# Optimization experiments

Measured on AMD Instinct MI355X. Metric: run time of the kernel, lower is better.

Reference implementation:

```python
import jax, jax.numpy as jnp
import numpy as np

B, NV, NC, D, GD = 4, 2048, 8192, 64, 8


def setup_inputs() -> dict:
    key = jax.random.key(0)
    ks = jax.random.split(key, 16)
    f32 = jnp.float32
    rn = lambda k, s, fan: (jax.random.normal(k, s, dtype=f32) / np.float32(np.sqrt(fan)))
    raw = jax.random.randint(ks[0], (B, NC, NV), 0, 20)
    c_mat = jnp.where(raw == 0, -1.0, jnp.where(raw == 1, 1.0, 0.0)).astype(f32)
    v_mat = jnp.transpose(c_mat, (0, 2, 1))  # [B, NV, NC]
    variables = jax.random.normal(ks[1], (B, NV, D), dtype=f32)
    ground_vars = jax.random.normal(ks[2], (B, NV, GD), dtype=f32)
    # learned params
    c_block = rn(ks[3], (2, D, D), D)  # pos/neg literal projections (clause side)
    v_block = rn(ks[4], (2, D, D), D)  # pos/neg literal projections (variable side)
    vb = jax.random.normal(ks[5], (D,), dtype=f32)
    cb = jax.random.normal(ks[6], (D,), dtype=f32)
    Wg = rn(ks[7], (D, GD + D), GD + D)  # ground combiner Linear(concat) -> D
    bg = jnp.zeros((D,), f32)
    Wz = rn(ks[8], (D, D), D); Uz = rn(ks[9], (D, D), D); bz = jnp.zeros((D,), f32)
    Wr = rn(ks[10], (D, D), D); Ur = rn(ks[11], (D, D), D); br = jnp.zeros((D,), f32)
    Wh = rn(ks[12], (D, D), D); Uh = rn(ks[13], (D, D), D); bh = jnp.zeros((D,), f32)
    return dict(variables=variables, ground_vars=ground_vars, c_mat=c_mat, v_mat=v_mat,
                c_block=c_block, v_block=v_block, vb=vb, cb=cb, Wg=Wg, bg=bg,
                Wz=Wz, Uz=Uz, bz=bz, Wr=Wr, Ur=Ur, br=br, Wh=Wh, Uh=Uh, bh=bh)


def reference(variables, ground_vars, c_mat, v_mat, c_block, v_block, vb, cb,
              Wg, bg, Wz, Uz, bz, Wr, Ur, br, Wh, Uh, bh):
    b, nv, d = variables.shape
    v = variables.reshape(-1, d)  # [B*NV, D]
    # clause-side literal projections: bmm(c_block, v^T)^T == v @ c_block[i]^T
    pos_vars = (v @ c_block[0].T).reshape(b, nv, d)
    neg_vars = (v @ c_block[1].T).reshape(b, nv, d)
    pos_cmat = jnp.clip(c_mat, 0.0, 1.0)
    neg_cmat = -jnp.clip(c_mat, -1.0, 0.0)
    c = (jnp.einsum('bcv,bvd->bcd', pos_cmat, pos_vars)
         + jnp.einsum('bcv,bvd->bcd', neg_cmat, neg_vars))  # [B, NC, D]
    c = jax.nn.relu(c + cb)
    cv = c.reshape(-1, d)  # [B*NC, D]
    pos_cvars = (cv @ v_block[0].T).reshape(b, -1, d)
    neg_cvars = (cv @ v_block[1].T).reshape(b, -1, d)
    pos_vmat = jnp.clip(v_mat, 0.0, 1.0)
    neg_vmat = -jnp.clip(v_mat, -1.0, 0.0)
    nv_msg = (jnp.einsum('bvc,bcd->bvd', pos_vmat, pos_cvars)
              + jnp.einsum('bvc,bcd->bvd', neg_vmat, neg_cvars))  # [B, NV, D]
    v_emb = jax.nn.relu(nv_msg + vb).reshape(-1, d)
    # ground combiner: tanh(Linear(concat(ground, v_emb)))
    g = ground_vars.reshape(-1, ground_vars.shape[-1])
    av = jnp.tanh(jnp.concatenate([g, v_emb], axis=-1) @ Wg.T + bg)
    # GRU update against previous variable embeddings
    prev = v
    z = jax.nn.sigmoid(av @ Wz.T + prev @ Uz.T + bz)
    r = jax.nn.sigmoid(av @ Wr.T + prev @ Ur.T + br)
    h_tilda = jnp.tanh(av @ Wh.T + (r * prev) @ Uh.T + bh)
    h = (1.0 - z) * prev + z * h_tilda
    return h.reshape(b, nv * d, 1)
```

## Files before the change

kernel.cpp:

```cpp
#include <hip/hip_runtime.h>
#include <hip/hip_bf16.h>
#include <stdint.h>

#define NBATCH 4
#define NV 2048
#define NC 8192
#define DD 64

typedef __attribute__((ext_vector_type(8))) short s16x8;
typedef __attribute__((ext_vector_type(4))) float fx4;
typedef __attribute__((ext_vector_type(8))) unsigned short u16x8;
typedef __attribute__((ext_vector_type(4))) int i32x4;
typedef __attribute__((ext_vector_type(2))) unsigned int u32x2;

static __device__ __forceinline__ void gload_lds16(const void* g, void* l) {
    __builtin_amdgcn_global_load_lds(
        (const __attribute__((address_space(1))) unsigned int*)g,
        (__attribute__((address_space(3))) unsigned int*)l, 16, 0, 0);
}

__global__ __launch_bounds__(256) void k_front(
    const float* __restrict__ cmat, unsigned short* __restrict__ comp,
    const float* __restrict__ vars, const float* __restrict__ cblk,
    char* __restrict__ qsh, char* __restrict__ qsl,
    char* __restrict__ qdh, char* __restrict__ qdl)
{
    __shared__ __align__(16) char pool[41472];
    int blk = blockIdx.x;
    int t = threadIdx.x;
    if (blk < 4096) {
        char (*sb)[260] = (char(*)[260])pool;
        int tv = blk & 7;
        int rg = (blk >> 3) & 127;
        int b = blk >> 10;
        int wv = t >> 6, l = t & 63;
        int crow0 = rg * 64;
        const float* src = cmat + (size_t)b * NC * NV + (size_t)crow0 * NV + tv * 256;
        #pragma unroll 4
        for (int rr = 0; rr < 16; ++rr) {
            int r = wv * 16 + rr;
            fx4 x = *(const fx4*)(src + (size_t)r * NV + l * 4);
            unsigned int pk = ((unsigned int)((int)x[0] & 0xFF))
                            | (((unsigned int)((int)x[1] & 0xFF)) << 8)
                            | (((unsigned int)((int)x[2] & 0xFF)) << 16)
                            | (((unsigned int)((int)x[3] & 0xFF)) << 24);
            *(unsigned int*)&sb[r][l * 4] = pk;
        }
        __syncthreads();
        unsigned short* cbp = comp + ((size_t)b * 256 + tv * 32) * NC + crow0;
        #pragma unroll
        for (int it = 0; it < 8; ++it) {
            int idx = it * 256 + t;
            int v8l = idx >> 6, r = idx & 63;
            unsigned int lo = *(const unsigned int*)&sb[r][v8l * 8];
            unsigned int hi = *(const unsigned int*)&sb[r][v8l * 8 + 4];
            unsigned int c0 = 0;
            #pragma unroll
            for (int i = 0; i < 4; ++i) c0 |= ((lo >> (8 * i)) & 3u) << (2 * i);
            #pragma unroll
            for (int i = 0; i < 4; ++i) c0 |= ((hi >> (8 * i)) & 3u) << (8 + 2 * i);
            cbp[(size_t)v8l * NC + r] = (unsigned short)c0;
        }
    } else {
        float (*sv)[64] = (float(*)[64])pool;
        float (*scb)[65] = (float(*)[65])(pool + 8192);
        int blk2 = blk - 4096;
        int b = blk2 >> 6, ch = blk2 & 63;
        const float* vsrc = vars + ((size_t)b * NV + (size_t)ch * 32) * DD;
        for (int i = t; i < 32 * 64; i += 256) sv[i >> 6][i & 63] = vsrc[i];
        for (int i = t; i < 2 * 64 * 64; i += 256) {
            int pn = i >> 12, dout = (i >> 6) & 63, k = i & 63;
            scb[pn * 64 + k][dout] = cblk[i];
        }
        __syncthreads();
        int ks = t >> 6, dout = t & 63;
        unsigned int wsh[2] = {0, 0}, wsl[2] = {0, 0}, wdh[2] = {0, 0}, wdl[2] = {0, 0};
        #pragma unroll
        for (int c8 = 0; c8 < 8; ++c8) {
            int vloc = ks * 8 + c8;
            float ap = 0.f, an = 0.f;
            for (int k = 0; k < 64; ++k) {
                float vv = sv[vloc][k];
                ap += vv * scb[k][dout];
                an += vv * scb[64 + k][dout];
            }
            float s = (ap + an) * 0.5f, dv = (ap - an) * 0.5f;
            int qs_ = (int)rintf(s * 4096.f);
            int qd_ = (int)rintf(dv * 4096.f);
            qs_ = min(max(qs_, -32511), 32511);
            qd_ = min(max(qd_, -32511), 32511);
            int sh = (qs_ + 128) >> 8, sl = qs_ - (sh << 8);
            int dh = (qd_ + 128) >> 8, dl = qd_ - (dh << 8);
            int w = c8 >> 2, sft = (c8 & 3) * 8;
            wsh[w] |= (unsigned int)(sh & 0xFF) << sft;
            wsl[w] |= (unsigned int)(sl & 0xFF) << sft;
            wdh[w] |= (unsigned int)(dh & 0xFF) << sft;
            wdl[w] |= (unsigned int)(dl & 0xFF) << sft;
        }
        int kc = ch >> 1;
        int lg = ((ch & 1) << 1) | (ks >> 1);
        size_t off = (((size_t)(b * 32 + kc) * 64 + dout) * 4 + lg) * 16 + (ks & 1) * 8;
        *(u32x2*)(qsh + off) = (u32x2){wsh[0], wsh[1]};
        *(u32x2*)(qsl + off) = (u32x2){wsl[0], wsl[1]};
        *(u32x2*)(qdh + off) = (u32x2){wdh[0], wdh[1]};
        *(u32x2*)(qdl + off) = (u32x2){wdl[0], wdl[1]};
    }
}

__global__ __launch_bounds__(256, 2) void k_phaseA(
    const unsigned short* __restrict__ comp,
    const char* __restrict__ qsh, const char* __restrict__ qsl,
    const char* __restrict__ qdh, const char* __restrict__ qdl,
    const float* __restrict__ cb, const float* __restrict__ vblk,
    char* __restrict__ csh, char* __restrict__ csl,
    char* __restrict__ cdh, char* __restrict__ cdl)
{
    __shared__ __align__(16) char pool[50176];
    int blk = blockIdx.x;
    int b = blk & 3;
    int rg = blk >> 2;
    int t = threadIdx.x;
    int wv = t >> 6, l = t & 63, lr = l & 15, lg = l >> 4;
    int crow0 = rg * 64;
    int crow = crow0 + wv * 16 + lr;
    const unsigned short* compb = comp + (size_t)b * 256 * NC;

    i32x4 ahi[4], alo[4];
    #pragma unroll
    for (int n = 0; n < 4; ++n) { ahi[n] = (i32x4){0,0,0,0}; alo[n] = (i32x4){0,0,0,0}; }

    {
        size_t gb = ((size_t)(b * 32)) * 4096 + (size_t)t * 16;
        char* lp = pool + t * 16;
        gload_lds16(qsh + gb, lp);
        gload_lds16(qsl + gb, lp + 4096);
        gload_lds16(qdh + gb, lp + 8192);
        gload_lds16(qdl + gb, lp + 12288);
    }
    unsigned int u0, u1, u0n, u1n;
    u0 = compb[(size_t)(lg * 2) * NC + crow];
    u1 = compb[(size_t)(lg * 2 + 1) * NC + crow];
    __syncthreads();

    int cur = 0;
    #pragma unroll 1
    for (int kc = 0; kc < 32; ++kc) {
        if (kc < 31) {
            size_t gb = ((size_t)(b * 32 + kc + 1)) * 4096 + (size_t)t * 16;
            char* lp = pool + (cur ^ 1) * 16384 + t * 16;
            gload_lds16(qsh + gb, lp);
            gload_lds16(qsl + gb, lp + 4096);
            gload_lds16(qdh + gb, lp + 8192);
            gload_lds16(qdl + gb, lp + 12288);
            size_t v8 = (size_t)((kc + 1) * 8 + lg * 2);
            u0n = compb[v8 * NC + crow];
            u1n = compb[(v8 + 1) * NC + crow];
        }
        i32x4 Asgn, Aabs;
        #pragma unroll
        for (int w = 0; w < 4; ++w) {
            unsigned int wg = 0;
            #pragma unroll
            for (int jj = 0; jj < 4; ++jj) {
                int j = w * 4 + jj;
                unsigned int u = (j < 8) ? u0 : u1;
                int c = ((int)(u << (30 - 2 * (j & 7)))) >> 30;
                wg |= ((unsigned int)c & 0xFFu) << (8 * jj);
            }
            Asgn[w] = (int)wg;
        }
        #pragma unroll
        for (int w = 0; w < 4; ++w) Aabs[w] = Asgn[w] & 0x01010101;
        const char* bufp = pool + cur * 16384;
        #pragma unroll
        for (int n = 0; n < 4; ++n) {
            int boff = ((n * 16 + lr) * 4 + lg) * 16;
            i32x4 Bsh = *(const i32x4*)(bufp + boff);
            i32x4 Bsl = *(const i32x4*)(bufp + 4096 + boff);
            i32x4 Bdh = *(const i32x4*)(bufp + 8192 + boff);
            i32x4 Bdl = *(const i32x4*)(bufp + 12288 + boff);
            ahi[n] = __builtin_amdgcn_mfma_i32_16x16x64_i8(Aabs, Bsh, ahi[n], 0, 0, 0);
            ahi[n] = __builtin_amdgcn_mfma_i32_16x16x64_i8(Asgn, Bdh, ahi[n], 0, 0, 0);
            alo[n] = __builtin_amdgcn_mfma_i32_16x16x64_i8(Aabs, Bsl, alo[n], 0, 0, 0);
            alo[n] = __builtin_amdgcn_mfma_i32_16x16x64_i8(Asgn, Bdl, alo[n], 0, 0, 0);
        }
        if (kc < 31) { u0 = u0n; u1 = u1n; }
        __syncthreads();
        cur ^= 1;
    }

    int* sbC = (int*)pool;
    float* sbCf = (float*)pool;
    float* svb = (float*)(pool + 64 * 66 * 4);
    #pragma unroll
    for (int n = 0; n < 4; ++n)
        #pragma unroll
        for (int r = 0; r < 4; ++r)
            sbC[(wv * 16 + lg * 4 + r) * 66 + n * 16 + lr] = ahi[n][r] * 256 + alo[n][r];
    for (int i = t * 4; i < 8192; i += 1024) {
        fx4 g4 = *(const fx4*)(vblk + i);
        int pn = i >> 12, dout = (i >> 6) & 63, k0 = i & 63;
        #pragma unroll
        for (int jj = 0; jj < 4; ++jj) svb[(pn * 64 + k0 + jj) * 65 + dout] = g4[jj];
    }
    __syncthreads();
    for (int idx = t; idx < 4096; idx += 256) {
        int row = idx >> 6, k = idx & 63;
        float f = (float)sbC[row * 66 + k] * (1.0f / 4096.0f) + cb[k];
        sbCf[row * 66 + k] = fmaxf(f, 0.f);
    }
    __syncthreads();
    int dout = l;
    float ap[16], an[16];
    #pragma unroll
    for (int c8 = 0; c8 < 16; ++c8) { ap[c8] = 0.f; an[c8] = 0.f; }
    for (int k = 0; k < 64; ++k) {
        float w0 = svb[k * 65 + dout];
        float w1 = svb[(64 + k) * 65 + dout];
        #pragma unroll
        for (int c8 = 0; c8 < 16; ++c8) {
            float rc = sbCf[(wv * 16 + c8) * 66 + k];
            ap[c8] += rc * w0;
            an[c8] += rc * w1;
        }
    }
    unsigned int osh[4] = {0,0,0,0}, osl[4] = {0,0,0,0}, odh[4] = {0,0,0,0}, odl[4] = {0,0,0,0};
    #pragma unroll
    for (int c8 = 0; c8 < 16; ++c8) {
        float s = (ap[c8] + an[c8]) * 0.5f, dv = (ap[c8] - an[c8]) * 0.5f;
        int q_s = (int)rintf(s * 512.f);
        int q_d = (int)rintf(dv * 512.f);
        q_s = min(max(q_s, -32511), 32511);
        q_d = min(max(q_d, -32511), 32511);
        int sh = (q_s + 128) >> 8, sl = q_s - (sh << 8);
        int dh = (q_d + 128) >> 8, dl = q_d - (dh << 8);
        int w = c8 >> 2, sft = (c8 & 3) * 8;
        osh[w] |= (unsigned int)(sh & 0xFF) << sft;
        osl[w] |= (unsigned int)(sl & 0xFF) << sft;
        odh[w] |= (unsigned int)(dh & 0xFF) << sft;
        odl[w] |= (unsigned int)(dl & 0xFF) << sft;
    }
    size_t off = (((size_t)(b * 128 + rg) * 64 + dout) * 64) + wv * 16;
    *(i32x4*)(csh + off) = (i32x4){(int)osh[0], (int)osh[1], (int)osh[2], (int)osh[3]};
    *(i32x4*)(csl + off) = (i32x4){(int)osl[0], (int)osl[1], (int)osl[2], (int)osl[3]};
    *(i32x4*)(cdh + off) = (i32x4){(int)odh[0], (int)odh[1], (int)odh[2], (int)odh[3]};
    *(i32x4*)(cdl + off) = (i32x4){(int)odl[0], (int)odl[1], (int)odl[2], (int)odl[3]};
}

__global__ __launch_bounds__(256, 4) void k_phaseB(
    const unsigned short* __restrict__ comp,
    const char* __restrict__ csh, const char* __restrict__ csl,
    const char* __restrict__ cdh, const char* __restrict__ cdl,
    float* __restrict__ npart)
{
    __shared__ char lds[2][16384];
    int blk = blockIdx.x;
    int combo = blk & 63;
    int rg = blk >> 6;
    int b = combo >> 4;
    int q = combo & 15;
    int t = threadIdx.x;
    int wv = t >> 6, l = t & 63, lr = l & 15, lg = l >> 4;
    int v0 = rg * 128 + wv * 32;
    const unsigned short* compb = comp + (size_t)b * 256 * NC;
    int sh_ = 2 * (lr & 7);
    const unsigned short* cp0 = compb + (size_t)((v0 + lr) >> 3) * NC + q * 512 + lg * 16;
    const unsigned short* cp1 = compb + (size_t)((v0 + 16 + lr) >> 3) * NC + q * 512 + lg * 16;
    const size_t cbase = ((size_t)(b * 128 + q * 8)) * 4096;

    i32x4 ahi[2][4], alo[2][4];
    #pragma unroll
    for (int i = 0; i < 2; ++i)
        #pragma unroll
        for (int j = 0; j < 4; ++j) { ahi[i][j] = (i32x4){0,0,0,0}; alo[i][j] = (i32x4){0,0,0,0}; }

    {
        size_t gb = cbase + (size_t)t * 16;
        char* lp = &lds[0][t * 16];
        gload_lds16(csh + gb, lp);
        gload_lds16(csl + gb, lp + 4096);
        gload_lds16(cdh + gb, lp + 8192);
        gload_lds16(cdl + gb, lp + 12288);
    }
    __syncthreads();

    int cur = 0;
    #pragma unroll 1
    for (int cc = 0; cc < 8; ++cc) {
        u16x8 u00 = *(const u16x8*)(cp0 + cc * 64);
        u16x8 u01 = *(const u16x8*)(cp0 + cc * 64 + 8);
        u16x8 u10 = *(const u16x8*)(cp1 + cc * 64);
        u16x8 u11 = *(const u16x8*)(cp1 + cc * 64 + 8);
        if (cc < 7) {
            size_t gb = cbase + (size_t)(cc + 1) * 4096 + (size_t)t * 16;
            char* lp = &lds[cur ^ 1][t * 16];
            gload_lds16(csh + gb, lp);
            gload_lds16(csl + gb, lp + 4096);
            gload_lds16(cdh + gb, lp + 8192);
            gload_lds16(cdl + gb, lp + 12288);
        }
        i32x4 Asgn[2], Aabs[2];
        #pragma unroll
        for (int rt = 0; rt < 2; ++rt) {
            u16x8 ua = rt ? u10 : u00;
            u16x8 ub = rt ? u11 : u01;
            i32x4 sg;
            #pragma unroll
            for (int g = 0; g < 4; ++g) {
                unsigned int wg = 0;
                #pragma unroll
                for (int jj = 0; jj < 4; ++jj) {
                    int j = g * 4 + jj;
                    unsigned int code = ((unsigned int)(j < 8 ? ua[j & 7] : ub[j & 7]) >> sh_) & 3u;
                    unsigned int byt = (code == 3u) ? 0xFFu : code;
                    wg |= byt << (jj * 8);
                }
                sg[g] = (int)wg;
            }
            Asgn[rt] = sg;
            i32x4 ab;
            #pragma unroll
            for (int g = 0; g < 4; ++g) ab[g] = sg[g] & 0x01010101;
            Aabs[rt] = ab;
        }
        const char* bufp = &lds[cur][0];
        #pragma unroll
        for (int n = 0; n < 4; ++n) {
            int boff = ((n * 16 + lr) * 4 + lg) * 16;
            i32x4 Bsh = *(const i32x4*)(bufp + boff);
            i32x4 Bsl = *(const i32x4*)(bufp + 4096 + boff);
            i32x4 Bdh = *(const i32x4*)(bufp + 8192 + boff);
            i32x4 Bdl = *(const i32x4*)(bufp + 12288 + boff);
            #pragma unroll
            for (int rt = 0; rt < 2; ++rt) {
                ahi[rt][n] = __builtin_amdgcn_mfma_i32_16x16x64_i8(Aabs[rt], Bsh, ahi[rt][n], 0, 0, 0);
                ahi[rt][n] = __builtin_amdgcn_mfma_i32_16x16x64_i8(Asgn[rt], Bdh, ahi[rt][n], 0, 0, 0);
                alo[rt][n] = __builtin_amdgcn_mfma_i32_16x16x64_i8(Aabs[rt], Bsl, alo[rt][n], 0, 0, 0);
                alo[rt][n] = __builtin_amdgcn_mfma_i32_16x16x64_i8(Asgn[rt], Bdl, alo[rt][n], 0, 0, 0);
            }
        }
        __syncthreads();
        cur ^= 1;
    }
    float* dst = npart + (((size_t)q * NBATCH + b) * NV + v0) * DD;
    #pragma unroll
    for (int rt = 0; rt < 2; ++rt)
        #pragma unroll
        for (int n = 0; n < 4; ++n)
            #pragma unroll
            for (int r = 0; r < 4; ++r) {
                float v = (float)(ahi[rt][n][r] * 256 + alo[rt][n][r]) * (1.0f / 512.0f);
                dst[(size_t)(rt * 16 + lg * 4 + r) * DD + n * 16 + lr] = v;
            }
}

__global__ __launch_bounds__(512) void k_gru(
    const float* __restrict__ npart, const float* __restrict__ vars,
    const float* __restrict__ gv, const float* __restrict__ vb,
    const float* __restrict__ Wg, const float* __restrict__ bg,
    const float* __restrict__ Wz, const float* __restrict__ Uz, const float* __restrict__ bz,
    const float* __restrict__ Wr, const float* __restrict__ Ur, const float* __restrict__ brr,
    const float* __restrict__ Wh, const float* __restrict__ Uh, const float* __restrict__ bh,
    float* __restrict__ out)
{
    __shared__ float sWg[72][65];
    __shared__ float sWz[64][65], sUz[64][65];
    __shared__ float sWr[64][65], sUr[64][65];
    __shared__ float sWh[64][65], sUh[64][65];
    __shared__ float scat[8][72];
    __shared__ float sprev[8][64];
    __shared__ float sav[8][64];
    __shared__ float srp[8][64];
    int t = threadIdx.x;
    for (int i = t * 4; i < 4608; i += 2048) {
        fx4 g4 = *(const fx4*)(Wg + i);
        int dout = i / 72, j = i - dout * 72;
        #pragma unroll
        for (int jj = 0; jj < 4; ++jj) sWg[j + jj][dout] = g4[jj];
    }
    for (int i = t * 4; i < 4096; i += 2048) {
        int dout = i >> 6, k = i & 63;
        fx4 a;
        a = *(const fx4*)(Wz + i);
        #pragma unroll
        for (int jj = 0; jj < 4; ++jj) sWz[k + jj][dout] = a[jj];
        a = *(const fx4*)(Uz + i);
        #pragma unroll
        for (int jj = 0; jj < 4; ++jj) sUz[k + jj][dout] = a[jj];
        a = *(const fx4*)(Wr + i);
        #pragma unroll
        for (int jj = 0; jj < 4; ++jj) sWr[k + jj][dout] = a[jj];
        a = *(const fx4*)(Ur + i);
        #pragma unroll
        for (int jj = 0; jj < 4; ++jj) sUr[k + jj][dout] = a[jj];
        a = *(const fx4*)(Wh + i);
        #pragma unroll
        for (int jj = 0; jj < 4; ++jj) sWh[k + jj][dout] = a[jj];
        a = *(const fx4*)(Uh + i);
        #pragma unroll
        for (int jj = 0; jj < 4; ++jj) sUh[k + jj][dout] = a[jj];
    }
    int rr = t >> 6, dout = t & 63;
    const size_t qs = (size_t)NBATCH * NV * DD;
    #pragma unroll 1
    for (int it = 0; it < 4; ++it) {
        size_t row = (size_t)blockIdx.x * 32 + it * 8 + rr;
        float prev = vars[row * 64 + dout];
        float ve = vb[dout];
        #pragma unroll
        for (int s = 0; s < 16; ++s) ve += npart[(size_t)s * qs + row * 64 + dout];
        ve = fmaxf(ve, 0.f);
        scat[rr][8 + dout] = ve;
        if (dout < 8) scat[rr][dout] = gv[row * 8 + dout];
        sprev[rr][dout] = prev;
        __syncthreads();
        float a = bg[dout];
        for (int j = 0; j < 72; ++j) a += scat[rr][j] * sWg[j][dout];
        float av = 1.f - 2.f / (__expf(2.f * a) + 1.f);
        sav[rr][dout] = av;
        __syncthreads();
        float zi = bz[dout], ri = brr[dout], hwa = 0.f;
        for (int k = 0; k < 64; ++k) {
            float ak = sav[rr][k], pk = sprev[rr][k];
            zi += ak * sWz[k][dout] + pk * sUz[k][dout];
            ri += ak * sWr[k][dout] + pk * sUr[k][dout];
            hwa += ak * sWh[k][dout];
        }
        float z = 1.f / (1.f + __expf(-zi));
        float rgate = 1.f / (1.f + __expf(-ri));
        srp[rr][dout] = rgate * prev;
        __syncthreads();
        float hin = bh[dout] + hwa;
        for (int k = 0; k < 64; ++k) hin += srp[rr][k] * sUh[k][dout];
        float ht = 1.f - 2.f / (__expf(2.f * hin) + 1.f);
        out[row * 64 + dout] = (1.f - z) * prev + z * ht;
        __syncthreads();
    }
}

extern "C" void kernel_launch(void* const* d_in, const int* in_sizes, int n_in,
                              void* d_out, int out_size, void* d_ws, size_t ws_size,
                              hipStream_t stream) {
    (void)in_sizes; (void)n_in; (void)out_size; (void)ws_size;
    const float* vars = (const float*)d_in[0];
    const float* gv   = (const float*)d_in[1];
    const float* cmat = (const float*)d_in[2];
    const float* cblk = (const float*)d_in[4];
    const float* vblk = (const float*)d_in[5];
    const float* vb   = (const float*)d_in[6];
    const float* cb   = (const float*)d_in[7];
    const float* Wg   = (const float*)d_in[8];
    const float* bg   = (const float*)d_in[9];
    const float* Wz   = (const float*)d_in[10];
    const float* Uz   = (const float*)d_in[11];
    const float* bz   = (const float*)d_in[12];
    const float* Wr   = (const float*)d_in[13];
    const float* Ur   = (const float*)d_in[14];
    const float* br_  = (const float*)d_in[15];
    const float* Wh   = (const float*)d_in[16];
    const float* Uh   = (const float*)d_in[17];
    const float* bh   = (const float*)d_in[18];
    float* out = (float*)d_out;

    char* w = (char*)d_ws;
    const size_t MB = 1024 * 1024;
    char* qsh = w + 0 * MB;
    char* qsl = w + 1 * MB;
    char* qdh = w + 2 * MB;
    char* qdl = w + 3 * MB;
    char* csh = w + 4 * MB;
    char* csl = w + 6 * MB;
    char* cdh = w + 8 * MB;
    char* cdl = w + 10 * MB;
    float* npart         = (float*)(w + 12 * MB);
    unsigned short* comp = (unsigned short*)(w + 44 * MB);

    k_front<<<4352, 256, 0, stream>>>(cmat, comp, vars, cblk, qsh, qsl, qdh, qdl);
    k_phaseA<<<512, 256, 0, stream>>>(comp, qsh, qsl, qdh, qdl, cb, vblk,
                                      csh, csl, cdh, cdl);
    k_phaseB<<<1024, 256, 0, stream>>>(comp, csh, csl, cdh, cdl, npart);
    k_gru<<<256, 512, 0, stream>>>(npart, vars, gv, vb, Wg, bg,
                                   Wz, Uz, bz, Wr, Ur, br_, Wh, Uh, bh, out);
}
```

Baseline: 152.2 us.

## Use two waves per phaseA block, each computing two 16-row MFMA tiles

Phase A blocks drop from four waves to two, and each wave now handles 32 clause rows as two 16-row MFMA tiles. Each B fragment read from LDS then feeds twice as many MFMAs, and each thread issues twice as many global-to-LDS loads. The aim is fewer LDS reads per MFMA and less barrier cost per unit of work. In exchange, per-thread register pressure rises (double accumulators, 32-row epilogue arrays) and each block has fewer waves to hide latency.

Result: slower. 165.7 us (+8.9%).

```diff
diff --git a/kernel.cpp b/kernel.cpp
--- a/kernel.cpp
+++ b/kernel.cpp
@@ -107,7 +107,7 @@
     }
 }
 
-__global__ __launch_bounds__(256, 2) void k_phaseA(
+__global__ __launch_bounds__(128) void k_phaseA(
     const unsigned short* __restrict__ comp,
     const char* __restrict__ qsh, const char* __restrict__ qsl,
     const char* __restrict__ qdh, const char* __restrict__ qdl,
@@ -122,24 +122,31 @@
     int t = threadIdx.x;
     int wv = t >> 6, l = t & 63, lr = l & 15, lg = l >> 4;
     int crow0 = rg * 64;
-    int crow = crow0 + wv * 16 + lr;
+    int crow[2];
+    crow[0] = crow0 + wv * 32 + lr;
+    crow[1] = crow0 + wv * 32 + 16 + lr;
     const unsigned short* compb = comp + (size_t)b * 256 * NC;
 
-    i32x4 ahi[4], alo[4];
-    #pragma unroll
-    for (int n = 0; n < 4; ++n) { ahi[n] = (i32x4){0,0,0,0}; alo[n] = (i32x4){0,0,0,0}; }
+    i32x4 ahi[2][4], alo[2][4];
+    #pragma unroll
+    for (int rt = 0; rt < 2; ++rt)
+        #pragma unroll
+        for (int n = 0; n < 4; ++n) { ahi[rt][n] = (i32x4){0,0,0,0}; alo[rt][n] = (i32x4){0,0,0,0}; }
 
     {
         size_t gb = ((size_t)(b * 32)) * 4096 + (size_t)t * 16;
         char* lp = pool + t * 16;
-        gload_lds16(qsh + gb, lp);
-        gload_lds16(qsl + gb, lp + 4096);
-        gload_lds16(qdh + gb, lp + 8192);
-        gload_lds16(qdl + gb, lp + 12288);
-    }
-    unsigned int u0, u1, u0n, u1n;
-    u0 = compb[(size_t)(lg * 2) * NC + crow];
-    u1 = compb[(size_t)(lg * 2 + 1) * NC + crow];
+        gload_lds16(qsh + gb, lp);             gload_lds16(qsh + gb + 2048, lp + 2048);
+        gload_lds16(qsl + gb, lp + 4096);      gload_lds16(qsl + gb + 2048, lp + 6144);
+        gload_lds16(qdh + gb, lp + 8192);      gload_lds16(qdh + gb + 2048, lp + 10240);
+        gload_lds16(qdl + gb, lp + 12288);     gload_lds16(qdl + gb + 2048, lp + 14336);
+    }
+    unsigned int u0[2], u1[2], u0n[2], u1n[2];
+    #pragma unroll
+    for (int rt = 0; rt < 2; ++rt) {
+        u0[rt] = compb[(size_t)(lg * 2) * NC + crow[rt]];
+        u1[rt] = compb[(size_t)(lg * 2 + 1) * NC + crow[rt]];
+    }
     __syncthreads();
 
     int cur = 0;
@@ -148,29 +155,35 @@
         if (kc < 31) {
             size_t gb = ((size_t)(b * 32 + kc + 1)) * 4096 + (size_t)t * 16;
             char* lp = pool + (cur ^ 1) * 16384 + t * 16;
-            gload_lds16(qsh + gb, lp);
-            gload_lds16(qsl + gb, lp + 4096);
-            gload_lds16(qdh + gb, lp + 8192);
-            gload_lds16(qdl + gb, lp + 12288);
+            gload_lds16(qsh + gb, lp);             gload_lds16(qsh + gb + 2048, lp + 2048);
+            gload_lds16(qsl + gb, lp + 4096);      gload_lds16(qsl + gb + 2048, lp + 6144);
+            gload_lds16(qdh + gb, lp + 8192);      gload_lds16(qdh + gb + 2048, lp + 10240);
+            gload_lds16(qdl + gb, lp + 12288);     gload_lds16(qdl + gb + 2048, lp + 14336);
             size_t v8 = (size_t)((kc + 1) * 8 + lg * 2);
-            u0n = compb[v8 * NC + crow];
-            u1n = compb[(v8 + 1) * NC + crow];
-        }
-        i32x4 Asgn, Aabs;
-        #pragma unroll
-        for (int w = 0; w < 4; ++w) {
-            unsigned int wg = 0;
-            #pragma unroll
-            for (int jj = 0; jj < 4; ++jj) {
-                int j = w * 4 + jj;
-                unsigned int u = (j < 8) ? u0 : u1;
-                int c = ((int)(u << (30 - 2 * (j & 7)))) >> 30;
-                wg |= ((unsigned int)c & 0xFFu) << (8 * jj);
-            }
-            Asgn[w] = (int)wg;
-        }
-        #pragma unroll
-        for (int w = 0; w < 4; ++w) Aabs[w] = Asgn[w] & 0x01010101;
+            #pragma unroll
+            for (int rt = 0; rt < 2; ++rt) {
+                u0n[rt] = compb[v8 * NC + crow[rt]];
+                u1n[rt] = compb[(v8 + 1) * NC + crow[rt]];
+            }
+        }
+        i32x4 Asgn[2], Aabs[2];
+        #pragma unroll
+        for (int rt = 0; rt < 2; ++rt) {
+            #pragma unroll
+            for (int w = 0; w < 4; ++w) {
+                unsigned int wg = 0;
+                #pragma unroll
+                for (int jj = 0; jj < 4; ++jj) {
+                    int j = w * 4 + jj;
+                    unsigned int u = (j < 8) ? u0[rt] : u1[rt];
+                    int c = ((int)(u << (30 - 2 * (j & 7)))) >> 30;
+                    wg |= ((unsigned int)c & 0xFFu) << (8 * jj);
+                }
+                Asgn[rt][w] = (int)wg;
+            }
+            #pragma unroll
+            for (int w = 0; w < 4; ++w) Aabs[rt][w] = Asgn[rt][w] & 0x01010101;
+        }
         const char* bufp = pool + cur * 16384;
         #pragma unroll
         for (int n = 0; n < 4; ++n) {
@@ -179,12 +192,18 @@
             i32x4 Bsl = *(const i32x4*)(bufp + 4096 + boff);
             i32x4 Bdh = *(const i32x4*)(bufp + 8192 + boff);
             i32x4 Bdl = *(const i32x4*)(bufp + 12288 + boff);
-            ahi[n] = __builtin_amdgcn_mfma_i32_16x16x64_i8(Aabs, Bsh, ahi[n], 0, 0, 0);
-            ahi[n] = __builtin_amdgcn_mfma_i32_16x16x64_i8(Asgn, Bdh, ahi[n], 0, 0, 0);
-            alo[n] = __builtin_amdgcn_mfma_i32_16x16x64_i8(Aabs, Bsl, alo[n], 0, 0, 0);
-            alo[n] = __builtin_amdgcn_mfma_i32_16x16x64_i8(Asgn, Bdl, alo[n], 0, 0, 0);
-        }
-        if (kc < 31) { u0 = u0n; u1 = u1n; }
+            #pragma unroll
+            for (int rt = 0; rt < 2; ++rt) {
+                ahi[rt][n] = __builtin_amdgcn_mfma_i32_16x16x64_i8(Aabs[rt], Bsh, ahi[rt][n], 0, 0, 0);
+                ahi[rt][n] = __builtin_amdgcn_mfma_i32_16x16x64_i8(Asgn[rt], Bdh, ahi[rt][n], 0, 0, 0);
+                alo[rt][n] = __builtin_amdgcn_mfma_i32_16x16x64_i8(Aabs[rt], Bsl, alo[rt][n], 0, 0, 0);
+                alo[rt][n] = __builtin_amdgcn_mfma_i32_16x16x64_i8(Asgn[rt], Bdl, alo[rt][n], 0, 0, 0);
+            }
+        }
+        if (kc < 31) {
+            #pragma unroll
+            for (int rt = 0; rt < 2; ++rt) { u0[rt] = u0n[rt]; u1[rt] = u1n[rt]; }
+        }
         __syncthreads();
         cur ^= 1;
     }
@@ -193,40 +212,45 @@
     float* sbCf = (float*)pool;
     float* svb = (float*)(pool + 64 * 66 * 4);
     #pragma unroll
-    for (int n = 0; n < 4; ++n)
-        #pragma unroll
-        for (int r = 0; r < 4; ++r)
-            sbC[(wv * 16 + lg * 4 + r) * 66 + n * 16 + lr] = ahi[n][r] * 256 + alo[n][r];
-    for (int i = t * 4; i < 8192; i += 1024) {
+    for (int rt = 0; rt < 2; ++rt)
+        #pragma unroll
+        for (int n = 0; n < 4; ++n)
+            #pragma unroll
+            for (int r = 0; r < 4; ++r)
+                sbC[(wv * 32 + rt * 16 + lg * 4 + r) * 66 + n * 16 + lr] =
+                    ahi[rt][n][r] * 256 + alo[rt][n][r];
+    for (int i = t * 4; i < 8192; i += 512) {
         fx4 g4 = *(const fx4*)(vblk + i);
         int pn = i >> 12, dout = (i >> 6) & 63, k0 = i & 63;
         #pragma unroll
         for (int jj = 0; jj < 4; ++jj) svb[(pn * 64 + k0 + jj) * 65 + dout] = g4[jj];
     }
     __syncthreads();
-    for (int idx = t; idx < 4096; idx += 256) {
+    for (int idx = t; idx < 4096; idx += 128) {
         int row = idx >> 6, k = idx & 63;
         float f = (float)sbC[row * 66 + k] * (1.0f / 4096.0f) + cb[k];
         sbCf[row * 66 + k] = fmaxf(f, 0.f);
     }
     __syncthreads();
     int dout = l;
-    float ap[16], an[16];
-    #pragma unroll
-    for (int c8 = 0; c8 < 16; ++c8) { ap[c8] = 0.f; an[c8] = 0.f; }
+    float ap[32], an[32];
+    #pragma unroll
+    for (int c8 = 0; c8 < 32; ++c8) { ap[c8] = 0.f; an[c8] = 0.f; }
     for (int k = 0; k < 64; ++k) {
         float w0 = svb[k * 65 + dout];
         float w1 = svb[(64 + k) * 65 + dout];
         #pragma unroll
-        for (int c8 = 0; c8 < 16; ++c8) {
-            float rc = sbCf[(wv * 16 + c8) * 66 + k];
+        for (int c8 = 0; c8 < 32; ++c8) {
+            float rc = sbCf[(wv * 32 + c8) * 66 + k];
             ap[c8] += rc * w0;
             an[c8] += rc * w1;
         }
     }
-    unsigned int osh[4] = {0,0,0,0}, osl[4] = {0,0,0,0}, odh[4] = {0,0,0,0}, odl[4] = {0,0,0,0};
-    #pragma unroll
-    for (int c8 = 0; c8 < 16; ++c8) {
+    unsigned int osh[8], osl[8], odh[8], odl[8];
+    #pragma unroll
+    for (int w = 0; w < 8; ++w) { osh[w] = 0; osl[w] = 0; odh[w] = 0; odl[w] = 0; }
+    #pragma unroll
+    for (int c8 = 0; c8 < 32; ++c8) {
         float s = (ap[c8] + an[c8]) * 0.5f, dv = (ap[c8] - an[c8]) * 0.5f;
         int q_s = (int)rintf(s * 512.f);
         int q_d = (int)rintf(dv * 512.f);
@@ -240,11 +264,14 @@
         odh[w] |= (unsigned int)(dh & 0xFF) << sft;
         odl[w] |= (unsigned int)(dl & 0xFF) << sft;
     }
-    size_t off = (((size_t)(b * 128 + rg) * 64 + dout) * 64) + wv * 16;
-    *(i32x4*)(csh + off) = (i32x4){(int)osh[0], (int)osh[1], (int)osh[2], (int)osh[3]};
-    *(i32x4*)(csl + off) = (i32x4){(int)osl[0], (int)osl[1], (int)osl[2], (int)osl[3]};
-    *(i32x4*)(cdh + off) = (i32x4){(int)odh[0], (int)odh[1], (int)odh[2], (int)odh[3]};
-    *(i32x4*)(cdl + off) = (i32x4){(int)odl[0], (int)odl[1], (int)odl[2], (int)odl[3]};
+    size_t off = (((size_t)(b * 128 + rg) * 64 + dout) * 64) + wv * 32;
+    #pragma unroll
+    for (int h = 0; h < 2; ++h) {
+        *(i32x4*)(csh + off + h * 16) = (i32x4){(int)osh[h*4], (int)osh[h*4+1], (int)osh[h*4+2], (int)osh[h*4+3]};
+        *(i32x4*)(csl + off + h * 16) = (i32x4){(int)osl[h*4], (int)osl[h*4+1], (int)osl[h*4+2], (int)osl[h*4+3]};
+        *(i32x4*)(cdh + off + h * 16) = (i32x4){(int)odh[h*4], (int)odh[h*4+1], (int)odh[h*4+2], (int)odh[h*4+3]};
+        *(i32x4*)(cdl + off + h * 16) = (i32x4){(int)odl[h*4], (int)odl[h*4+1], (int)odl[h*4+2], (int)odl[h*4+3]};
+    }
 }
 
 __global__ __launch_bounds__(256, 4) void k_phaseB(
@@ -476,7 +503,7 @@
     unsigned short* comp = (unsigned short*)(w + 44 * MB);
 
     k_front<<<4352, 256, 0, stream>>>(cmat, comp, vars, cblk, qsh, qsl, qdh, qdl);
-    k_phaseA<<<512, 256, 0, stream>>>(comp, qsh, qsl, qdh, qdl, cb, vblk,
+    k_phaseA<<<512, 128, 0, stream>>>(comp, qsh, qsl, qdh, qdl, cb, vblk,
                                       csh, csl, cdh, cdl);
     k_phaseB<<<1024, 256, 0, stream>>>(comp, csh, csl, cdh, cdl, npart);
     k_gru<<<256, 512, 0, stream>>>(npart, vars, gv, vb, Wg, bg,
```
